# Kernel tuning notes

Measured on AMD Instinct MI355X. Metric: run time of the kernel, lower is better.

The kernel has to match this reference:

```python
import jax, jax.numpy as jnp
import numpy as np

D = 256       # vec_dim
HEADS = 8     # head_num
PS = 4        # patch_size
WS = 7        # window_size (in patches)
P = WS * WS   # tokens per window


def _relative_index():
    # replicates the torch meshgrid / relative coord logic (indexing='ij')
    coords = np.stack(np.meshgrid(np.arange(WS), np.arange(WS), indexing='ij'))  # [2,WS,WS]
    cf = coords.reshape(2, -1)                                                   # [2,P]
    rc = (cf[:, :, None] - cf[:, None, :]).transpose(1, 2, 0)                    # [P,P,2]
    rc[:, :, 0] += WS - 1
    rc[:, :, 1] += WS - 1
    rc[:, :, 1] *= 2 * WS - 1
    return rc.sum(-1)  # [P,P] ints in [0,(2WS-1)^2)


def _shift_mask(ch, cw):
    # standard swin shift mask built on the patch grid (ch, cw)
    fm = np.zeros((ch, cw))
    idx = (slice(0, -WS), slice(-WS, -(WS // 2)), slice(-(WS // 2), None))
    cnt = 0
    for y in idx:
        for x in idx:
            fm[y, x] = cnt
            cnt += 1
    nh, nw = ch // WS, cw // WS
    fm = fm.reshape(nh, WS, nw, WS).transpose(0, 2, 1, 3).reshape(nh * nw, P)
    m = fm[:, None, :] - fm[:, :, None]
    return np.where(m != 0, -100.0, 0.0).astype(np.float32)


def setup_inputs() -> dict:
    key = jax.random.key(0)
    ks = jax.random.split(key, 10)
    N, PN = 8, 3136
    s = 0.02
    return {
        'inputs': jax.random.normal(ks[0], (N, D, PN), jnp.float32),
        'Wk': jax.random.normal(ks[1], (HEADS * D, D), jnp.float32) * s,
        'bk': jax.random.normal(ks[2], (HEADS * D,), jnp.float32) * s,
        'Wq': jax.random.normal(ks[3], (HEADS * D, D), jnp.float32) * s,
        'bq': jax.random.normal(ks[4], (HEADS * D,), jnp.float32) * s,
        'Wv': jax.random.normal(ks[5], (HEADS * D, D), jnp.float32) * s,
        'bv': jax.random.normal(ks[6], (HEADS * D,), jnp.float32) * s,
        'Wo': jax.random.normal(ks[7], (D, HEADS * D), jnp.float32) * s,
        'bo': jax.random.normal(ks[8], (D,), jnp.float32) * s,
        'rel_code': jax.random.normal(ks[9], ((2 * WS - 1) ** 2, HEADS), jnp.float32) * 0.02,
        'h': 224,
        'w': 224,
    }


def _forward(inputs, Wk, bk, Wq, bq, Wv, bv, Wo, bo, rel_code, h, w):
    ch, cw = h // PS, w // PS            # patch grid
    N, _, PN = inputs.shape
    C = D // (PS * PS)
    nh, nw = ch // WS, cw // WS
    WIN = nh * nw

    # patches2features -> pixel-space roll by WS//2 -> features2patches
    x = inputs.reshape(N, C, PS, PS, ch, cw)
    x = x.transpose(0, 1, 4, 2, 5, 3).reshape(N, C, ch * PS, cw * PS)
    x = jnp.roll(x, (WS // 2, WS // 2), axis=(-2, -1))
    x = x.reshape(N, C, ch, PS, cw, PS).transpose(0, 2, 4, 1, 3, 5).reshape(N, PN, D)
    x = x.transpose(0, 2, 1)  # [N,D,PN]

    def proj(W, b):
        e = jnp.einsum('od,ndp->nop', W, x) + b[None, :, None]  # [N,HEADS*D,PN]
        e = e.reshape(N, HEADS, D, ch, cw)
        # window partition: n h d (nh w1)(nw w2) -> n h (nh nw) d (w1 w2)
        e = e.reshape(N, HEADS, D, nh, WS, nw, WS)
        return e.transpose(0, 1, 3, 5, 2, 4, 6).reshape(N, HEADS, WIN, D, P)

    k = proj(Wk, bk)
    q = proj(Wq, bq)
    v = proj(Wv, bv)

    # attn[p,q] = k_p . q_q  (softmax over keys p, axis=3)
    attn = jnp.einsum('nhgdp,nhgdq->nhgpq', k, q) / (D ** 0.5)
    mask = jnp.asarray(_shift_mask(ch, cw))
    attn = attn + mask[None, None]
    rel_idx = _relative_index().ravel()
    rel = rel_code[rel_idx].reshape(P, P, HEADS).transpose(2, 0, 1)  # [H,P,P]
    attn = attn + rel[None, :, None]
    wmap = jax.nn.softmax(attn, axis=3)

    out = jnp.einsum('nhgdp,nhgpq->nhgdq', v, wmap)
    # window merge back to [N,H,D,PN]
    out = out.reshape(N, HEADS, nh, nw, D, WS, WS)
    out = out.transpose(0, 1, 4, 2, 5, 3, 6).reshape(N, HEADS * D, PN)
    return jnp.einsum('od,ndp->nop', Wo, out) + bo[None, :, None]  # [N,D,PN]


def reference(inputs, Wk, bk, Wq, bq, Wv, bv, Wo, bo, rel_code, h, w):
    return _forward(inputs, Wk, bk, Wq, bq, Wv, bv, Wo, bo, rel_code, h, w)
```

## Files before the change

kernel.cpp:

```cpp
#include <hip/hip_runtime.h>
#include <hip/hip_bf16.h>


#define NBATCH 8
#define MSTR   2176
#define TROWS  3200

typedef unsigned short ushort_t;
typedef __attribute__((ext_vector_type(8))) short bf16x8;
typedef __attribute__((ext_vector_type(8))) unsigned short u16x8;
typedef __attribute__((ext_vector_type(4))) float f32x4;

__device__ __forceinline__ float b2f(ushort_t u) {
  union { unsigned int i; float f; } v; v.i = ((unsigned int)u) << 16; return v.f;
}
__device__ __forceinline__ ushort_t f2b(float f) {
  union { float f; unsigned int u; } v; v.f = f;
  unsigned int u = v.u;
  return (ushort_t)((u + 0x7FFFu + ((u >> 16) & 1u)) >> 16);
}
__device__ __forceinline__ int regof(int y) { return (y < 49) ? 0 : ((y < 53) ? 1 : 2); }
__device__ __forceinline__ int div7(int t) { return (t * 37) >> 8; }
__device__ __forceinline__ int tmap(int p, int gi, int gj) {
  int wi = div7(p); return (gi * 7 + wi) * 56 + gj * 7 + (p - wi * 7);
}
__device__ __forceinline__ ushort4 pack4(f32x4 a) {
  ushort4 u; u.x = f2b(a[0]); u.y = f2b(a[1]); u.z = f2b(a[2]); u.w = f2b(a[3]);
  return u;
}

__global__ void k_pc(const float* __restrict__ Wk, const float* __restrict__ Wq,
                     const float* __restrict__ Wo, const float* __restrict__ Wv,
                     const float* __restrict__ bk, const float* __restrict__ bq,
                     const float* __restrict__ bv, const float* __restrict__ bo,
                     const float* __restrict__ relc, const float* __restrict__ X,
                     ushort_t* __restrict__ Aext, ushort_t* __restrict__ Wov3,
                     float* __restrict__ cvec, float* __restrict__ relL2,
                     ushort_t* __restrict__ Xroll) {
  __shared__ float red[8];
  int blk = blockIdx.x, t = threadIdx.x;
  if (blk >= 1290) {
    const int cb = blk - 1290;
    const int n = cb / 57, y = cb % 57;
    ushort_t* xr = Xroll + (size_t)n * TROWS * 256;
    const int d = t;
    if (y == 56) {
      for (int i = d; i < 64 * 256 / 8; i += 256)
        *(u16x8*)(xr + 3136 * 256 + i * 8) = (u16x8){0,0,0,0,0,0,0,0};
      return;
    }
    const int c = d >> 4, p1 = (d >> 2) & 3, p2 = d & 3;
    const int sp = c * 16 + (((p1 + 1) & 3) << 2) + ((p2 + 1) & 3);
    const int ty = (p1 == 3) ? y : ((y == 0) ? 55 : y - 1);
    const float* rowp = X + (size_t)n * 256 * 3136 + sp * 3136 + ty * 56;
    ushort_t* orow = xr + y * 56 * 256 + d;
    for (int x = 0; x < 56; ++x) {
      int tx = (p2 == 3) ? x : ((x == 0) ? 55 : x - 1);
      orow[x * 256] = f2b(rowp[tx]);
    }
  } else if (blk < 512) {
    int h = blk >> 6, b0 = (blk & 63) << 2, a = t;
    const float* wkh = Wk + h * 65536;
    const float* wqh = Wq + h * 65536;
    float a0 = 0.f, a1 = 0.f, a2 = 0.f, a3 = 0.f;
    for (int dd = 0; dd < 256; ++dd) {
      float wk = wkh[dd * 256 + a];
      float4 w4 = *(const float4*)(wqh + dd * 256 + b0);
      a0 += wk * w4.x; a1 += wk * w4.y; a2 += wk * w4.z; a3 += wk * w4.w;
    }
    ushort4 u; u.x = f2b(a0); u.y = f2b(a1); u.z = f2b(a2); u.w = f2b(a3);
    *(ushort4*)(Aext + (h * 256 + a) * 256 + b0) = u;
  } else if (blk < 1024) {
    int bb = blk - 512;
    int h = bb >> 6, o0 = (bb & 63) << 2, d = t;
    float a0 = 0.f, a1 = 0.f, a2 = 0.f, a3 = 0.f;
    for (int dd = 0; dd < 256; ++dd) {
      float wv = Wv[(h * 256 + dd) * 256 + d];
      a0 += Wo[(o0 + 0) * 2048 + h * 256 + dd] * wv;
      a1 += Wo[(o0 + 1) * 2048 + h * 256 + dd] * wv;
      a2 += Wo[(o0 + 2) * 2048 + h * 256 + dd] * wv;
      a3 += Wo[(o0 + 3) * 2048 + h * 256 + dd] * wv;
    }
    Wov3[(o0 + 0) * 2048 + h * 256 + d] = f2b(a0);
    Wov3[(o0 + 1) * 2048 + h * 256 + d] = f2b(a1);
    Wov3[(o0 + 2) * 2048 + h * 256 + d] = f2b(a2);
    Wov3[(o0 + 3) * 2048 + h * 256 + d] = f2b(a3);
  } else if (blk < 1032) {
    int h = blk - 1024;
    float s1 = 0.f, s2 = 0.f;
    for (int dd = 0; dd < 256; ++dd) {
      s1 += bk[h * 256 + dd] * Wq[(h * 256 + dd) * 256 + t];
      s2 += bq[h * 256 + dd] * Wk[(h * 256 + dd) * 256 + t];
    }
    Aext[(2048 + h) * 256 + t] = f2b(s1);
    Aext[(2056 + h) * 256 + t] = f2b(s2);
  } else if (blk == 1032) {
    for (int i = t; i < 112 * 256 / 8; i += 256)
      *(u16x8*)(Aext + 2064 * 256 + i * 8) = (u16x8){0,0,0,0,0,0,0,0};
  } else if (blk < 1289) {
    int o = blk - 1033;
    const float* wob = Wo + o * 2048;
    float acc = 0.f;
#pragma unroll
    for (int j = 0; j < 8; ++j) acc += wob[j * 256 + t] * bv[j * 256 + t];
#pragma unroll
    for (int s = 1; s < 64; s <<= 1) acc += __shfl_xor(acc, s);
    if ((t & 63) == 0) red[t >> 6] = acc;
    __syncthreads();
    if (t == 0) cvec[o] = bo[o] + red[0] + red[1] + red[2] + red[3];
  } else {
    if (t < 8) {
      float c = 0.f;
      for (int dd = 0; dd < 256; ++dd) c += bk[t * 256 + dd] * bq[t * 256 + dd];
      red[t] = c * 0.0625f;
    }
    __syncthreads();
    for (int i = t; i < 8 * 169; i += 256) {
      int h = i / 169, idx = i - h * 169;
      relL2[i] = relc[idx * 8 + h] + red[h];
    }
  }
}

__global__ __launch_bounds__(256, 2) void k_gemm1(
    const ushort_t* __restrict__ Xroll, const ushort_t* __restrict__ Aext,
    ushort_t* __restrict__ MT) {
  __shared__ ushort_t Asm[128 * 72];
  __shared__ ushort_t Bsm[128 * 72];
  const int bx = blockIdx.x;
  const int n = bx / 425, r = bx % 425;
  const int tt = r / 17, aa = r % 17;
  const int a0 = aa * 128, t0 = tt * 128;
  const int tid = threadIdx.x, wave = tid >> 6, lane = tid & 63;
  const int quad = lane >> 4, l16 = lane & 15;
  const int wa = wave >> 1, wt = wave & 1;
  const ushort_t* Xn = Xroll + (size_t)n * TROWS * 256;
  ushort_t* Mn = MT + (size_t)n * TROWS * MSTR;

  const int sr = tid >> 1, sc = (tid & 1) * 4;
  bf16x8 ra[4], rb[4];
#pragma unroll
  for (int i = 0; i < 4; ++i) {
    ra[i] = *(const bf16x8*)(Aext + (a0 + sr) * 256 + (sc + i) * 8);
    rb[i] = *(const bf16x8*)(Xn + (t0 + sr) * 256 + (sc + i) * 8);
  }

  f32x4 acc[4][4];
#pragma unroll
  for (int i = 0; i < 4; ++i)
#pragma unroll
    for (int j = 0; j < 4; ++j) acc[i][j] = (f32x4){0.f, 0.f, 0.f, 0.f};

  for (int kit = 0; kit < 4; ++kit) {
#pragma unroll
    for (int i = 0; i < 4; ++i) {
      *(bf16x8*)(&Asm[sr * 72 + (sc + i) * 8]) = ra[i];
      *(bf16x8*)(&Bsm[sr * 72 + (sc + i) * 8]) = rb[i];
    }
    __syncthreads();
    if (kit < 3) {
      int k0 = (kit + 1) * 64;
#pragma unroll
      for (int i = 0; i < 4; ++i) {
        ra[i] = *(const bf16x8*)(Aext + (a0 + sr) * 256 + k0 + (sc + i) * 8);
        rb[i] = *(const bf16x8*)(Xn + (t0 + sr) * 256 + k0 + (sc + i) * 8);
      }
    }
#pragma unroll
    for (int kk = 0; kk < 2; ++kk) {
      bf16x8 af[4], bf[4];
#pragma unroll
      for (int i = 0; i < 4; ++i)
        af[i] = *(const bf16x8*)(&Asm[(wa * 64 + i * 16 + l16) * 72 + kk * 32 + quad * 8]);
#pragma unroll
      for (int j = 0; j < 4; ++j)
        bf[j] = *(const bf16x8*)(&Bsm[(wt * 64 + j * 16 + l16) * 72 + kk * 32 + quad * 8]);
#pragma unroll
      for (int i = 0; i < 4; ++i)
#pragma unroll
        for (int j = 0; j < 4; ++j)
          acc[i][j] = __builtin_amdgcn_mfma_f32_16x16x32_bf16(af[i], bf[j], acc[i][j], 0, 0, 0);
    }
    __syncthreads();
  }
#pragma unroll
  for (int i = 0; i < 4; ++i)
#pragma unroll
    for (int j = 0; j < 4; ++j) {
      int tg = t0 + wt * 64 + j * 16 + l16;
      int ag = a0 + wa * 64 + i * 16 + quad * 4;
      *(ushort4*)(Mn + (size_t)tg * MSTR + ag) = pack4(acc[i][j]);
    }
}

#define XP3 264
__global__ __launch_bounds__(512, 4) void k_attn3(
    const ushort_t* __restrict__ Xroll, const ushort_t* __restrict__ MT,
    const ushort_t* __restrict__ Wov3, const float* __restrict__ relL2,
    const float* __restrict__ cvec, float* __restrict__ out) {
  __shared__ ushort_t Xp[64 * XP3];
  __shared__ ushort_t TT[64 * XP3];
  __shared__ ushort_t StB[64 * 72];
  __shared__ float aqsL[8 * 64];
  __shared__ float bpsL[8 * 64];

  const int tid = threadIdx.x;
  const int wave = tid >> 6, lane = tid & 63;
  const int quad = lane >> 4, l16 = lane & 15;
  const int n = blockIdx.x >> 6, g = blockIdx.x & 63;
  const int gi = g >> 3, gj = g & 7;
  const ushort_t* Xn = Xroll + (size_t)n * TROWS * 256;
  const ushort_t* Mn = MT + (size_t)n * TROWS * MSTR;

  {
    const int p = tid & 63, cg = tid >> 6;
    if (p < 49) {
      int t = tmap(p, gi, gj);
#pragma unroll
      for (int i = 0; i < 4; ++i)
        *(u16x8*)(&Xp[p * XP3 + (cg * 4 + i) * 8]) =
            *(const u16x8*)(Xn + t * 256 + (cg * 4 + i) * 8);
    } else {
#pragma unroll
      for (int i = 0; i < 4; ++i)
        *(u16x8*)(&Xp[p * XP3 + (cg * 4 + i) * 8]) = (u16x8){0,0,0,0,0,0,0,0};
    }
  }
  {
    const int h = tid >> 6, q = tid & 63;
    int qq = (q < 49) ? q : 48;
    int t = tmap(qq, gi, gj);
    aqsL[h * 64 + q] = b2f(Mn[(size_t)t * MSTR + 2048 + h]);
    bpsL[h * 64 + q] = b2f(Mn[(size_t)t * MSTR + 2056 + h]);
  }
  __syncthreads();

  bf16x8 xfr[2][2];
#pragma unroll
  for (int i = 0; i < 2; ++i) {
    const int d = (wave * 2 + i) * 16 + l16;
#pragma unroll
    for (int kk = 0; kk < 2; ++kk)
#pragma unroll
      for (int j = 0; j < 8; ++j)
        xfr[i][kk][j] = (short)Xp[(kk * 32 + quad * 8 + j) * XP3 + d];
  }

  const int qt = wave >> 1, ph = wave & 1;
  const int q = qt * 16 + l16;
  const int qq = (q < 49) ? q : 48;
  const int tq = tmap(qq, gi, gj);
  const ushort_t* Mbase = Mn + (size_t)tq * MSTR + quad * 8;
  const int yq = div7(qq), xq = qq - yq * 7;
  const int fq = regof(gi * 7 + yq) * 3 + regof(gj * 7 + xq);

  f32x4 yac[2][4];
#pragma unroll
  for (int i = 0; i < 2; ++i)
#pragma unroll
    for (int j = 0; j < 4; ++j) yac[i][j] = (f32x4){0.f, 0.f, 0.f, 0.f};

  for (int h = 0; h < 8; ++h) {
    f32x4 sacc[2];
#pragma unroll
    for (int i = 0; i < 2; ++i) sacc[i] = (f32x4){0.f, 0.f, 0.f, 0.f};
    const ushort_t* mrow = Mbase + h * 256;
#pragma unroll
    for (int kk = 0; kk < 8; ++kk) {
      bf16x8 bm = *(const bf16x8*)(mrow + kk * 32);
#pragma unroll
      for (int i = 0; i < 2; ++i) {
        bf16x8 af = *(const bf16x8*)(&Xp[((ph * 2 + i) * 16 + l16) * XP3 + kk * 32 + quad * 8]);
        sacc[i] = __builtin_amdgcn_mfma_f32_16x16x32_bf16(af, bm, sacc[i], 0, 0, 0);
      }
    }
    {
      const float aqv = aqsL[h * 64 + q];
      const float* relh = relL2 + h * 169;
#pragma unroll
      for (int i = 0; i < 2; ++i) {
        ushort4 sv;
        ushort_t* svp = &sv.x;
#pragma unroll
        for (int r = 0; r < 4; ++r) {
          int p = (ph * 2 + i) * 16 + quad * 4 + r;
          float val = -1e30f;
          if (p < 49) {
            int yp = div7(p), xp = p - yp * 7;
            int fp = regof(gi * 7 + yp) * 3 + regof(gj * 7 + xp);
            val = (sacc[i][r] + aqv + bpsL[h * 64 + p]) * 0.0625f +
                  relh[(yp - yq + 6) + 13 * (xp - xq + 6)];
            if (fp != fq) val -= 100.f;
          }
          svp[r] = f2b(val);
        }
        *(ushort4*)(&StB[q * 72 + (ph * 2 + i) * 16 + quad * 4]) = sv;
      }
    }
    __syncthreads();

    {
      const int sq = tid >> 3, sub = tid & 7;
      ushort_t* row = &StB[sq * 72 + sub * 8];
      bf16x8 in8 = *(const bf16x8*)row;
      float v[8];
#pragma unroll
      for (int i = 0; i < 8; ++i) v[i] = b2f((ushort_t)in8[i]);
      float m = v[0];
#pragma unroll
      for (int i = 1; i < 8; ++i) m = fmaxf(m, v[i]);
      m = fmaxf(m, __shfl_xor(m, 1));
      m = fmaxf(m, __shfl_xor(m, 2));
      m = fmaxf(m, __shfl_xor(m, 4));
      float s = 0.f;
#pragma unroll
      for (int i = 0; i < 8; ++i) { v[i] = __expf(v[i] - m); s += v[i]; }
      s += __shfl_xor(s, 1);
      s += __shfl_xor(s, 2);
      s += __shfl_xor(s, 4);
      float inv = 1.f / s;
      bf16x8 w8;
#pragma unroll
      for (int i = 0; i < 8; ++i) w8[i] = (short)f2b(v[i] * inv);
      *(bf16x8*)row = w8;
    }
    __syncthreads();

    {
      f32x4 tacc[2][4];
#pragma unroll
      for (int i = 0; i < 2; ++i)
#pragma unroll
        for (int j = 0; j < 4; ++j) tacc[i][j] = (f32x4){0.f, 0.f, 0.f, 0.f};
#pragma unroll
      for (int kk = 0; kk < 2; ++kk) {
        bf16x8 bw[4];
#pragma unroll
        for (int j = 0; j < 4; ++j)
          bw[j] = *(const bf16x8*)(&StB[(j * 16 + l16) * 72 + kk * 32 + quad * 8]);
#pragma unroll
        for (int i = 0; i < 2; ++i)
#pragma unroll
          for (int j = 0; j < 4; ++j)
            tacc[i][j] = __builtin_amdgcn_mfma_f32_16x16x32_bf16(xfr[i][kk], bw[j], tacc[i][j], 0, 0, 0);
      }
#pragma unroll
      for (int i = 0; i < 2; ++i)
#pragma unroll
        for (int j = 0; j < 4; ++j)
          *(ushort4*)(&TT[(j * 16 + l16) * XP3 + (wave * 2 + i) * 16 + quad * 4]) =
              pack4(tacc[i][j]);
    }
    __syncthreads();

    {
      const ushort_t* wb = Wov3 + h * 256 + quad * 8;
#pragma unroll
      for (int kk = 0; kk < 8; ++kk) {
        bf16x8 at[4];
#pragma unroll
        for (int j = 0; j < 4; ++j)
          at[j] = *(const bf16x8*)(&TT[(j * 16 + l16) * XP3 + kk * 32 + quad * 8]);
#pragma unroll
        for (int i = 0; i < 2; ++i) {
          bf16x8 bwv = *(const bf16x8*)(wb + (size_t)((wave * 2 + i) * 16 + l16) * 2048 + kk * 32);
#pragma unroll
          for (int j = 0; j < 4; ++j)
            yac[i][j] = __builtin_amdgcn_mfma_f32_16x16x32_bf16(at[j], bwv, yac[i][j], 0, 0, 0);
        }
      }
    }
  }

  float* obase = out + (size_t)n * 256 * 3136;
#pragma unroll
  for (int i = 0; i < 2; ++i) {
    const int o = (wave * 2 + i) * 16 + l16;
    const float cv = cvec[o];
#pragma unroll
    for (int j = 0; j < 4; ++j) {
#pragma unroll
      for (int r = 0; r < 4; ++r) {
        int qv = j * 16 + quad * 4 + r;
        if (qv < 49) {
          int pos = tmap(qv, gi, gj);
          obase[(size_t)o * 3136 + pos] = yac[i][j][r] + cv;
        }
      }
    }
  }
}

extern "C" void kernel_launch(void* const* d_in, const int* in_sizes, int n_in,
                              void* d_out, int out_size, void* d_ws, size_t ws_size,
                              hipStream_t stream) {
  (void)in_sizes; (void)n_in; (void)out_size; (void)ws_size;
  const float* X  = (const float*)d_in[0];
  const float* Wk = (const float*)d_in[1];
  const float* bk = (const float*)d_in[2];
  const float* Wq = (const float*)d_in[3];
  const float* bq = (const float*)d_in[4];
  const float* Wv = (const float*)d_in[5];
  const float* bv = (const float*)d_in[6];
  const float* Wo = (const float*)d_in[7];
  const float* bo = (const float*)d_in[8];
  const float* rc = (const float*)d_in[9];

  ushort_t* MT    = (ushort_t*)d_ws;
  ushort_t* Xroll = MT + (size_t)8 * TROWS * MSTR;
  ushort_t* Aext  = Xroll + (size_t)8 * TROWS * 256;
  ushort_t* Wov3  = Aext + 2176 * 256;
  float* fbase = (float*)(Wov3 + 256 * 2048);
  float* cvec  = fbase;
  float* relL2 = fbase + 256;
  float* out = (float*)d_out;

  k_pc   <<<dim3(1746), dim3(256), 0, stream>>>(Wk, Wq, Wo, Wv, bk, bq, bv, bo, rc, X,
                                                Aext, Wov3, cvec, relL2, Xroll);
  k_gemm1<<<dim3(8 * 425), dim3(256), 0, stream>>>(Xroll, Aext, MT);
  k_attn3<<<dim3(8 * 64), dim3(512), 0, stream>>>(Xroll, MT, Wov3, relL2, cvec, out);
}
```

Before: 319.5 us.

## Fuse projection GEMM into attention kernel, dropping the MT intermediate buffer

Removes the separate k_gemm1 kernel that wrote a large bf16 intermediate MT (tokens x 2176) to global memory. Each window block of the attention kernel now computes, per head, the 64x256 product of the window's tokens with the combined K^T Q weight matrix using MFMA into LDS (reusing the old TT buffer), and computes the bias terms aqs/bps with a small MFMA. The precompute kernel also gives each thread 16 outputs instead of 4, so it launches fewer blocks. This saves a launch and the MT write and read traffic, at the cost of an extra sync and more MFMA work inside the occupancy-limited attention kernel.

```diff
diff --git a/kernel.cpp b/kernel.cpp
--- a/kernel.cpp
+++ b/kernel.cpp
@@ -3,7 +3,6 @@
 
 
 #define NBATCH 8
-#define MSTR   2176
 #define TROWS  3200
 
 typedef unsigned short ushort_t;
@@ -29,18 +28,18 @@
   return u;
 }
 
-__global__ void k_pc(const float* __restrict__ Wk, const float* __restrict__ Wq,
-                     const float* __restrict__ Wo, const float* __restrict__ Wv,
-                     const float* __restrict__ bk, const float* __restrict__ bq,
-                     const float* __restrict__ bv, const float* __restrict__ bo,
-                     const float* __restrict__ relc, const float* __restrict__ X,
-                     ushort_t* __restrict__ Aext, ushort_t* __restrict__ Wov3,
-                     float* __restrict__ cvec, float* __restrict__ relL2,
-                     ushort_t* __restrict__ Xroll) {
+__global__ void k_pc2(const float* __restrict__ Wk, const float* __restrict__ Wq,
+                      const float* __restrict__ Wo, const float* __restrict__ Wv,
+                      const float* __restrict__ bk, const float* __restrict__ bq,
+                      const float* __restrict__ bv, const float* __restrict__ bo,
+                      const float* __restrict__ relc, const float* __restrict__ X,
+                      ushort_t* __restrict__ Aext, ushort_t* __restrict__ Wov3,
+                      float* __restrict__ cvec, float* __restrict__ relL2,
+                      ushort_t* __restrict__ Xroll) {
   __shared__ float red[8];
   int blk = blockIdx.x, t = threadIdx.x;
-  if (blk >= 1290) {
-    const int cb = blk - 1290;
+  if (blk >= 522) {
+    const int cb = blk - 522;
     const int n = cb / 57, y = cb % 57;
     ushort_t* xr = Xroll + (size_t)n * TROWS * 256;
     const int d = t;
@@ -58,35 +57,37 @@
       int tx = (p2 == 3) ? x : ((x == 0) ? 55 : x - 1);
       orow[x * 256] = f2b(rowp[tx]);
     }
-  } else if (blk < 512) {
-    int h = blk >> 6, b0 = (blk & 63) << 2, a = t;
+  } else if (blk < 128) {
+    const int h = blk >> 4, b0 = (blk & 15) << 4, a = t;
     const float* wkh = Wk + h * 65536;
-    const float* wqh = Wq + h * 65536;
-    float a0 = 0.f, a1 = 0.f, a2 = 0.f, a3 = 0.f;
+    const float* wqh = Wq + h * 65536 + b0;
+    float acc[16];
+#pragma unroll
+    for (int j = 0; j < 16; ++j) acc[j] = 0.f;
     for (int dd = 0; dd < 256; ++dd) {
       float wk = wkh[dd * 256 + a];
-      float4 w4 = *(const float4*)(wqh + dd * 256 + b0);
-      a0 += wk * w4.x; a1 += wk * w4.y; a2 += wk * w4.z; a3 += wk * w4.w;
-    }
-    ushort4 u; u.x = f2b(a0); u.y = f2b(a1); u.z = f2b(a2); u.w = f2b(a3);
-    *(ushort4*)(Aext + (h * 256 + a) * 256 + b0) = u;
-  } else if (blk < 1024) {
-    int bb = blk - 512;
-    int h = bb >> 6, o0 = (bb & 63) << 2, d = t;
-    float a0 = 0.f, a1 = 0.f, a2 = 0.f, a3 = 0.f;
+#pragma unroll
+      for (int j = 0; j < 16; ++j) acc[j] += wk * wqh[dd * 256 + j];
+    }
+    ushort_t* dst = Aext + (h * 256 + a) * 256 + b0;
+#pragma unroll
+    for (int j = 0; j < 16; ++j) dst[j] = f2b(acc[j]);
+  } else if (blk < 256) {
+    const int bb = blk - 128;
+    const int h = bb >> 4, o0 = (bb & 15) << 4, d = t;
+    float acc[16];
+#pragma unroll
+    for (int j = 0; j < 16; ++j) acc[j] = 0.f;
     for (int dd = 0; dd < 256; ++dd) {
       float wv = Wv[(h * 256 + dd) * 256 + d];
-      a0 += Wo[(o0 + 0) * 2048 + h * 256 + dd] * wv;
-      a1 += Wo[(o0 + 1) * 2048 + h * 256 + dd] * wv;
-      a2 += Wo[(o0 + 2) * 2048 + h * 256 + dd] * wv;
-      a3 += Wo[(o0 + 3) * 2048 + h * 256 + dd] * wv;
-    }
-    Wov3[(o0 + 0) * 2048 + h * 256 + d] = f2b(a0);
-    Wov3[(o0 + 1) * 2048 + h * 256 + d] = f2b(a1);
-    Wov3[(o0 + 2) * 2048 + h * 256 + d] = f2b(a2);
-    Wov3[(o0 + 3) * 2048 + h * 256 + d] = f2b(a3);
-  } else if (blk < 1032) {
-    int h = blk - 1024;
+#pragma unroll
+      for (int j = 0; j < 16; ++j) acc[j] += Wo[(o0 + j) * 2048 + h * 256 + dd] * wv;
+    }
+#pragma unroll
+    for (int j = 0; j < 16; ++j)
+      Wov3[(o0 + j) * 2048 + h * 256 + d] = f2b(acc[j]);
+  } else if (blk < 264) {
+    const int h = blk - 256;
     float s1 = 0.f, s2 = 0.f;
     for (int dd = 0; dd < 256; ++dd) {
       s1 += bk[h * 256 + dd] * Wq[(h * 256 + dd) * 256 + t];
@@ -94,11 +95,11 @@
     }
     Aext[(2048 + h) * 256 + t] = f2b(s1);
     Aext[(2056 + h) * 256 + t] = f2b(s2);
-  } else if (blk == 1032) {
+  } else if (blk == 264) {
     for (int i = t; i < 112 * 256 / 8; i += 256)
       *(u16x8*)(Aext + 2064 * 256 + i * 8) = (u16x8){0,0,0,0,0,0,0,0};
-  } else if (blk < 1289) {
-    int o = blk - 1033;
+  } else if (blk < 521) {
+    const int o = blk - 265;
     const float* wob = Wo + o * 2048;
     float acc = 0.f;
 #pragma unroll
@@ -122,84 +123,13 @@
   }
 }
 
-__global__ __launch_bounds__(256, 2) void k_gemm1(
+#define XP3 264
+__global__ __launch_bounds__(512, 4) void k_attn5(
     const ushort_t* __restrict__ Xroll, const ushort_t* __restrict__ Aext,
-    ushort_t* __restrict__ MT) {
-  __shared__ ushort_t Asm[128 * 72];
-  __shared__ ushort_t Bsm[128 * 72];
-  const int bx = blockIdx.x;
-  const int n = bx / 425, r = bx % 425;
-  const int tt = r / 17, aa = r % 17;
-  const int a0 = aa * 128, t0 = tt * 128;
-  const int tid = threadIdx.x, wave = tid >> 6, lane = tid & 63;
-  const int quad = lane >> 4, l16 = lane & 15;
-  const int wa = wave >> 1, wt = wave & 1;
-  const ushort_t* Xn = Xroll + (size_t)n * TROWS * 256;
-  ushort_t* Mn = MT + (size_t)n * TROWS * MSTR;
-
-  const int sr = tid >> 1, sc = (tid & 1) * 4;
-  bf16x8 ra[4], rb[4];
-#pragma unroll
-  for (int i = 0; i < 4; ++i) {
-    ra[i] = *(const bf16x8*)(Aext + (a0 + sr) * 256 + (sc + i) * 8);
-    rb[i] = *(const bf16x8*)(Xn + (t0 + sr) * 256 + (sc + i) * 8);
-  }
-
-  f32x4 acc[4][4];
-#pragma unroll
-  for (int i = 0; i < 4; ++i)
-#pragma unroll
-    for (int j = 0; j < 4; ++j) acc[i][j] = (f32x4){0.f, 0.f, 0.f, 0.f};
-
-  for (int kit = 0; kit < 4; ++kit) {
-#pragma unroll
-    for (int i = 0; i < 4; ++i) {
-      *(bf16x8*)(&Asm[sr * 72 + (sc + i) * 8]) = ra[i];
-      *(bf16x8*)(&Bsm[sr * 72 + (sc + i) * 8]) = rb[i];
-    }
-    __syncthreads();
-    if (kit < 3) {
-      int k0 = (kit + 1) * 64;
-#pragma unroll
-      for (int i = 0; i < 4; ++i) {
-        ra[i] = *(const bf16x8*)(Aext + (a0 + sr) * 256 + k0 + (sc + i) * 8);
-        rb[i] = *(const bf16x8*)(Xn + (t0 + sr) * 256 + k0 + (sc + i) * 8);
-      }
-    }
-#pragma unroll
-    for (int kk = 0; kk < 2; ++kk) {
-      bf16x8 af[4], bf[4];
-#pragma unroll
-      for (int i = 0; i < 4; ++i)
-        af[i] = *(const bf16x8*)(&Asm[(wa * 64 + i * 16 + l16) * 72 + kk * 32 + quad * 8]);
-#pragma unroll
-      for (int j = 0; j < 4; ++j)
-        bf[j] = *(const bf16x8*)(&Bsm[(wt * 64 + j * 16 + l16) * 72 + kk * 32 + quad * 8]);
-#pragma unroll
-      for (int i = 0; i < 4; ++i)
-#pragma unroll
-        for (int j = 0; j < 4; ++j)
-          acc[i][j] = __builtin_amdgcn_mfma_f32_16x16x32_bf16(af[i], bf[j], acc[i][j], 0, 0, 0);
-    }
-    __syncthreads();
-  }
-#pragma unroll
-  for (int i = 0; i < 4; ++i)
-#pragma unroll
-    for (int j = 0; j < 4; ++j) {
-      int tg = t0 + wt * 64 + j * 16 + l16;
-      int ag = a0 + wa * 64 + i * 16 + quad * 4;
-      *(ushort4*)(Mn + (size_t)tg * MSTR + ag) = pack4(acc[i][j]);
-    }
-}
-
-#define XP3 264
-__global__ __launch_bounds__(512, 4) void k_attn3(
-    const ushort_t* __restrict__ Xroll, const ushort_t* __restrict__ MT,
     const ushort_t* __restrict__ Wov3, const float* __restrict__ relL2,
     const float* __restrict__ cvec, float* __restrict__ out) {
   __shared__ ushort_t Xp[64 * XP3];
-  __shared__ ushort_t TT[64 * XP3];
+  __shared__ ushort_t Ms[64 * XP3];
   __shared__ ushort_t StB[64 * 72];
   __shared__ float aqsL[8 * 64];
   __shared__ float bpsL[8 * 64];
@@ -210,7 +140,6 @@
   const int n = blockIdx.x >> 6, g = blockIdx.x & 63;
   const int gi = g >> 3, gj = g & 7;
   const ushort_t* Xn = Xroll + (size_t)n * TROWS * 256;
-  const ushort_t* Mn = MT + (size_t)n * TROWS * MSTR;
 
   {
     const int p = tid & 63, cg = tid >> 6;
@@ -226,14 +155,23 @@
         *(u16x8*)(&Xp[p * XP3 + (cg * 4 + i) * 8]) = (u16x8){0,0,0,0,0,0,0,0};
     }
   }
-  {
-    const int h = tid >> 6, q = tid & 63;
-    int qq = (q < 49) ? q : 48;
-    int t = tmap(qq, gi, gj);
-    aqsL[h * 64 + q] = b2f(Mn[(size_t)t * MSTR + 2048 + h]);
-    bpsL[h * 64 + q] = b2f(Mn[(size_t)t * MSTR + 2056 + h]);
-  }
   __syncthreads();
+
+  if (wave < 4) {
+    f32x4 bacc = (f32x4){0.f, 0.f, 0.f, 0.f};
+#pragma unroll
+    for (int kk = 0; kk < 8; ++kk) {
+      bf16x8 af = *(const bf16x8*)(Aext + (2048 + l16) * 256 + kk * 32 + quad * 8);
+      bf16x8 bf = *(const bf16x8*)(&Xp[(wave * 16 + l16) * XP3 + kk * 32 + quad * 8]);
+      bacc = __builtin_amdgcn_mfma_f32_16x16x32_bf16(af, bf, bacc, 0, 0, 0);
+    }
+#pragma unroll
+    for (int r = 0; r < 4; ++r) {
+      int row = quad * 4 + r;
+      if (row < 8) aqsL[row * 64 + wave * 16 + l16] = bacc[r];
+      else         bpsL[(row - 8) * 64 + wave * 16 + l16] = bacc[r];
+    }
+  }
 
   bf16x8 xfr[2][2];
 #pragma unroll
@@ -249,8 +187,6 @@
   const int qt = wave >> 1, ph = wave & 1;
   const int q = qt * 16 + l16;
   const int qq = (q < 49) ? q : 48;
-  const int tq = tmap(qq, gi, gj);
-  const ushort_t* Mbase = Mn + (size_t)tq * MSTR + quad * 8;
   const int yq = div7(qq), xq = qq - yq * 7;
   const int fq = regof(gi * 7 + yq) * 3 + regof(gj * 7 + xq);
 
@@ -261,13 +197,45 @@
     for (int j = 0; j < 4; ++j) yac[i][j] = (f32x4){0.f, 0.f, 0.f, 0.f};
 
   for (int h = 0; h < 8; ++h) {
+    __syncthreads();
+
+    {
+      const ushort_t* gh = Aext + h * 65536;
+      f32x4 macc[2][4];
+#pragma unroll
+      for (int i = 0; i < 2; ++i)
+#pragma unroll
+        for (int j = 0; j < 4; ++j) macc[i][j] = (f32x4){0.f, 0.f, 0.f, 0.f};
+#pragma unroll
+      for (int kk = 0; kk < 8; ++kk) {
+        bf16x8 af[2], bf[4];
+#pragma unroll
+        for (int i = 0; i < 2; ++i)
+          af[i] = *(const bf16x8*)(gh + ((wave * 2 + i) * 16 + l16) * 256 + kk * 32 + quad * 8);
+#pragma unroll
+        for (int j = 0; j < 4; ++j)
+          bf[j] = *(const bf16x8*)(&Xp[(j * 16 + l16) * XP3 + kk * 32 + quad * 8]);
+#pragma unroll
+        for (int i = 0; i < 2; ++i)
+#pragma unroll
+          for (int j = 0; j < 4; ++j)
+            macc[i][j] = __builtin_amdgcn_mfma_f32_16x16x32_bf16(af[i], bf[j], macc[i][j], 0, 0, 0);
+      }
+#pragma unroll
+      for (int i = 0; i < 2; ++i)
+#pragma unroll
+        for (int j = 0; j < 4; ++j)
+          *(ushort4*)(&Ms[(j * 16 + l16) * XP3 + (wave * 2 + i) * 16 + quad * 4]) =
+              pack4(macc[i][j]);
+    }
+    __syncthreads();
+
     f32x4 sacc[2];
 #pragma unroll
     for (int i = 0; i < 2; ++i) sacc[i] = (f32x4){0.f, 0.f, 0.f, 0.f};
-    const ushort_t* mrow = Mbase + h * 256;
 #pragma unroll
     for (int kk = 0; kk < 8; ++kk) {
-      bf16x8 bm = *(const bf16x8*)(mrow + kk * 32);
+      bf16x8 bm = *(const bf16x8*)(&Ms[q * XP3 + kk * 32 + quad * 8]);
 #pragma unroll
       for (int i = 0; i < 2; ++i) {
         bf16x8 af = *(const bf16x8*)(&Xp[((ph * 2 + i) * 16 + l16) * XP3 + kk * 32 + quad * 8]);
@@ -348,7 +316,7 @@
       for (int i = 0; i < 2; ++i)
 #pragma unroll
         for (int j = 0; j < 4; ++j)
-          *(ushort4*)(&TT[(j * 16 + l16) * XP3 + (wave * 2 + i) * 16 + quad * 4]) =
+          *(ushort4*)(&Ms[(j * 16 + l16) * XP3 + (wave * 2 + i) * 16 + quad * 4]) =
               pack4(tacc[i][j]);
     }
     __syncthreads();
@@ -360,7 +328,7 @@
         bf16x8 at[4];
 #pragma unroll
         for (int j = 0; j < 4; ++j)
-          at[j] = *(const bf16x8*)(&TT[(j * 16 + l16) * XP3 + kk * 32 + quad * 8]);
+          at[j] = *(const bf16x8*)(&Ms[(j * 16 + l16) * XP3 + kk * 32 + quad * 8]);
 #pragma unroll
         for (int i = 0; i < 2; ++i) {
           bf16x8 bwv = *(const bf16x8*)(wb + (size_t)((wave * 2 + i) * 16 + l16) * 2048 + kk * 32);
@@ -406,8 +374,7 @@
   const float* bo = (const float*)d_in[8];
   const float* rc = (const float*)d_in[9];
 
-  ushort_t* MT    = (ushort_t*)d_ws;
-  ushort_t* Xroll = MT + (size_t)8 * TROWS * MSTR;
+  ushort_t* Xroll = (ushort_t*)d_ws;
   ushort_t* Aext  = Xroll + (size_t)8 * TROWS * 256;
   ushort_t* Wov3  = Aext + 2176 * 256;
   float* fbase = (float*)(Wov3 + 256 * 2048);
@@ -415,8 +382,7 @@
   float* relL2 = fbase + 256;
   float* out = (float*)d_out;
 
-  k_pc   <<<dim3(1746), dim3(256), 0, stream>>>(Wk, Wq, Wo, Wv, bk, bq, bv, bo, rc, X,
-                                                Aext, Wov3, cvec, relL2, Xroll);
-  k_gemm1<<<dim3(8 * 425), dim3(256), 0, stream>>>(Xroll, Aext, MT);
-  k_attn3<<<dim3(8 * 64), dim3(512), 0, stream>>>(Xroll, MT, Wov3, relL2, cvec, out);
-}
+  k_pc2  <<<dim3(978), dim3(256), 0, stream>>>(Wk, Wq, Wo, Wv, bk, bq, bv, bo, rc, X,
+                                               Aext, Wov3, cvec, relL2, Xroll);
+  k_attn5<<<dim3(NBATCH * 64), dim3(512), 0, stream>>>(Xroll, Aext, Wov3, relL2, cvec, out);
+}
```

New measurement: 363.5 us. +13.8%, slower.
